# Kernel optimization log

Hardware: AMD Instinct MI355X
Metric: run time of the kernel (lower is better)

## Reference

```python
import jax, jax.numpy as jnp
import numpy as np

EPS = 1e-06

def _hermite_coeffs(coord_diff, sigmas):
    # coord_diff: [B,N,K,2], sigmas: [K] -> coeff: [B,N,K,6]
    dx = coord_diff[..., 0]  # [B,N,K]
    dy = coord_diff[..., 1]
    s2 = sigmas ** 2 + EPS   # [K], broadcasts over B,N
    s4 = sigmas ** 4 + EPS
    ones = jnp.ones_like(dx)
    # idx order follows nested (order, alpha) loop of the torch code:
    # (0,0), (0,1)->-dy, (1,0)->-dx, (0,2), (1,1), (2,0)
    coeff = jnp.stack([
        ones,
        -dy / s2,
        -dx / s2,
        dy ** 2 / s4 - 1.0 / s2,
        dx * dy / s4,
        dx ** 2 / s4 - 1.0 / s2,
    ], axis=-1)  # [B,N,K,6]
    return coeff


def setup_inputs() -> dict:
    key = jax.random.key(0)
    k1, k2, k3, k4, k5 = jax.random.split(key, 5)
    B, N, K, H, O = 4, 65536, 32, 6, 31
    return {
        "mlp_output": jax.random.normal(k1, (B, N, O), dtype=jnp.float32),
        "coord_diff": jax.random.normal(k2, (B, N, K, 2), dtype=jnp.float32),
        "sigmas": jax.random.uniform(k3, (K,), dtype=jnp.float32, minval=0.1, maxval=1.0),
        "gaussian_weights": jax.random.uniform(k4, (B, N, K), dtype=jnp.float32),
        "rbf_weights": jax.random.normal(k5, (K, H, O), dtype=jnp.float32),
    }


def reference(mlp_output, coord_diff, sigmas, gaussian_weights, rbf_weights):
    # final[b,n,o] = mlp_output[b,n,o] * sum_{k,h} coeff[b,n,k,h]*gw[b,n,k]*W[k,h,o]
    coeff = _hermite_coeffs(coord_diff, sigmas)            # [B,N,K,6]
    mix = jnp.einsum('bnkh,bnk,kho->bno', coeff, gaussian_weights, rbf_weights)
    return mlp_output * mix
```

## Files before the change

kernel.cpp:

```cpp
#include <hip/hip_runtime.h>

#define KK 32
#define HH 6
#define OO 31
#define EPS 1e-6f
#define PTS_BLK 256
#define V_DW (KK * 4 * HH * 8)

typedef float f32x16 __attribute__((ext_vector_type(16)));
typedef float f32x4  __attribute__((ext_vector_type(4)));

__device__ __align__(256) float V_dev[V_DW];

__global__ void hermite_prep_kernel(const float* __restrict__ W,
                                    const float* __restrict__ sigmas)
{
    int j = blockIdx.x * 256 + threadIdx.x;
    if (j >= V_DW) return;
    int k  = j / 192;
    int r  = j - k * 192;
    int oc = r / 48;
    int r2 = r - oc * 48;
    int h  = r2 >> 3;
    int o  = oc * 8 + (r2 & 7);
    float s  = sigmas[k];
    float s2 = s * s;
    float i2 = 1.0f / (s2 + EPS);
    float i4 = 1.0f / (s2 * s2 + EPS);
    float v = 0.0f;
    if (o < OO) {
        const float* Wk = W + k * (HH * OO);
        float w = Wk[h * OO + o];
        if (h == 0)      v = w - i2 * (Wk[3 * OO + o] + Wk[5 * OO + o]);
        else if (h <= 2) v = -i2 * w;
        else             v = i4 * w;
    }
    V_dev[j] = v;
}

#define CHUNK(PC, OCB)                                                     \
    {                                                                      \
        f32x16 t0, t1, t2;                                                 \
        asm volatile("s_load_dwordx16 %0, %3, 0x0\n\t"                     \
                     "s_load_dwordx16 %1, %3, 0x40\n\t"                    \
                     "s_load_dwordx16 %2, %3, 0x80\n\t"                    \
                     "s_waitcnt lgkmcnt(0)"                                \
                     : "=&s"(t0), "=&s"(t1), "=&s"(t2)                     \
                     : "s"(PC));                                           \
        _Pragma("unroll")                                                  \
        for (int o = 0; o < 8; ++o) {                                      \
            float a = acc[(OCB) + o];                                      \
            a = fmaf(g,  t0[o],     a);                                    \
            a = fmaf(d1, t0[8 + o], a);                                    \
            a = fmaf(d2, t1[o],     a);                                    \
            a = fmaf(d3, t1[8 + o], a);                                    \
            a = fmaf(d4, t2[o],     a);                                    \
            a = fmaf(d5, t2[8 + o], a);                                    \
            acc[(OCB) + o] = a;                                            \
        }                                                                  \
    }

#define JBLOCK(VS, GOFF)                                                   \
    _Pragma("unroll")                                                      \
    for (int j = 0; j < 8; ++j) {                                          \
        float dx = c[2 * j], dy = c[2 * j + 1];                            \
        float g  = ga[(GOFF) + j];                                         \
        float d1 = g * dy, d2 = g * dx;                                    \
        float d3 = d1 * dy, d4 = d1 * dx, d5 = d2 * dx;                    \
        const float* pk = (VS) + j * 192;                                  \
        CHUNK(pk,        0)                                                \
        CHUNK(pk + 48,   8)                                                \
        CHUNK(pk + 96,  16)                                                \
        CHUNK(pk + 144, 24)                                                \
    }

__global__ __launch_bounds__(256, 4) void hermite_fused_kernel(
    const float* __restrict__ mlp,
    const float* __restrict__ cd,
    const float* __restrict__ gw,
    float* __restrict__ out)
{
    __shared__ float smem[PTS_BLK * OO];

    const int tid = threadIdx.x;
    const int p   = blockIdx.x * PTS_BLK + tid;
    const float4* __restrict__ cdv = (const float4*)(cd + (size_t)p * (KK * 2));
    const float4* __restrict__ gwv = (const float4*)(gw + (size_t)p * KK);

    float acc[32];
#pragma unroll
    for (int o = 0; o < 32; ++o) acc[o] = 0.0f;

    const float* __restrict__ Vb = V_dev;

#pragma unroll 1
    for (int kt2 = 0; kt2 < 2; ++kt2) {
        float ga[16];
#pragma unroll
        for (int i = 0; i < 4; ++i) {
            float4 t = gwv[kt2 * 4 + i];
            ga[4 * i + 0] = t.x; ga[4 * i + 1] = t.y;
            ga[4 * i + 2] = t.z; ga[4 * i + 3] = t.w;
        }

        float c[16];
#pragma unroll
        for (int i = 0; i < 4; ++i) {
            float4 t = cdv[kt2 * 8 + i];
            c[4 * i + 0] = t.x; c[4 * i + 1] = t.y;
            c[4 * i + 2] = t.z; c[4 * i + 3] = t.w;
        }
        const float* Vs0 = Vb + (size_t)kt2 * (16 * 192);
        JBLOCK(Vs0, 0)

#pragma unroll
        for (int i = 0; i < 4; ++i) {
            float4 t = cdv[kt2 * 8 + 4 + i];
            c[4 * i + 0] = t.x; c[4 * i + 1] = t.y;
            c[4 * i + 2] = t.z; c[4 * i + 3] = t.w;
        }
        const float* Vs1 = Vs0 + 8 * 192;
        JBLOCK(Vs1, 8)
    }

#pragma unroll
    for (int o = 0; o < OO; ++o) smem[tid * OO + o] = acc[o];
    __syncthreads();

    {
        const size_t blk_dw = (size_t)blockIdx.x * (PTS_BLK * OO);
        const f32x4* __restrict__ mlpv = (const f32x4*)(mlp + blk_dw);
        f32x4* __restrict__ outv = (f32x4*)(out + blk_dw);
        const f32x4* mixv = (const f32x4*)smem;
#pragma unroll 2
        for (int j = tid; j < (PTS_BLK * OO) / 4; j += 256) {
            f32x4 m = __builtin_nontemporal_load(&mlpv[j]);
            f32x4 x = mixv[j];
            f32x4 r = m * x;
            __builtin_nontemporal_store(r, &outv[j]);
        }
    }
}

extern "C" void kernel_launch(void* const* d_in, const int* in_sizes, int n_in,
                              void* d_out, int out_size, void* d_ws, size_t ws_size,
                              hipStream_t stream)
{
    const float* mlp    = (const float*)d_in[0];
    const float* cd     = (const float*)d_in[1];
    const float* sigmas = (const float*)d_in[2];
    const float* gw     = (const float*)d_in[3];
    const float* W      = (const float*)d_in[4];
    float* out          = (float*)d_out;

    const int P = in_sizes[3] / KK;

    hermite_prep_kernel<<<(V_DW + 255) / 256, 256, 0, stream>>>(W, sigmas);
    hermite_fused_kernel<<<P / PTS_BLK, 256, 0, stream>>>(mlp, cd, gw, out);
}
```

Baseline: 199.3 us.

## Split output channels across waves so each wave handles four points per lane

Each wave now owns one 8-wide output-channel chunk of the precomputed weight table, and each lane computes four points instead of one. Each wave therefore issues only one set of 48 scalar loads per k and reuses them across four points, cutting scalar-load traffic and s_waitcnt stalls per FMA by about four times. In exchange every wave loads the coordinate and gaussian-weight inputs for all 256 points, so vector global reads rise roughly fourfold, though they should mostly hit in cache. The shared-memory write-out is remapped to the new point/channel layout.

Result: slower. 241.9 us (+21.3%).

```diff
diff --git a/kernel.cpp b/kernel.cpp
--- a/kernel.cpp
+++ b/kernel.cpp
@@ -38,42 +38,6 @@
     V_dev[j] = v;
 }
 
-#define CHUNK(PC, OCB)                                                     \
-    {                                                                      \
-        f32x16 t0, t1, t2;                                                 \
-        asm volatile("s_load_dwordx16 %0, %3, 0x0\n\t"                     \
-                     "s_load_dwordx16 %1, %3, 0x40\n\t"                    \
-                     "s_load_dwordx16 %2, %3, 0x80\n\t"                    \
-                     "s_waitcnt lgkmcnt(0)"                                \
-                     : "=&s"(t0), "=&s"(t1), "=&s"(t2)                     \
-                     : "s"(PC));                                           \
-        _Pragma("unroll")                                                  \
-        for (int o = 0; o < 8; ++o) {                                      \
-            float a = acc[(OCB) + o];                                      \
-            a = fmaf(g,  t0[o],     a);                                    \
-            a = fmaf(d1, t0[8 + o], a);                                    \
-            a = fmaf(d2, t1[o],     a);                                    \
-            a = fmaf(d3, t1[8 + o], a);                                    \
-            a = fmaf(d4, t2[o],     a);                                    \
-            a = fmaf(d5, t2[8 + o], a);                                    \
-            acc[(OCB) + o] = a;                                            \
-        }                                                                  \
-    }
-
-#define JBLOCK(VS, GOFF)                                                   \
-    _Pragma("unroll")                                                      \
-    for (int j = 0; j < 8; ++j) {                                          \
-        float dx = c[2 * j], dy = c[2 * j + 1];                            \
-        float g  = ga[(GOFF) + j];                                         \
-        float d1 = g * dy, d2 = g * dx;                                    \
-        float d3 = d1 * dy, d4 = d1 * dx, d5 = d2 * dx;                    \
-        const float* pk = (VS) + j * 192;                                  \
-        CHUNK(pk,        0)                                                \
-        CHUNK(pk + 48,   8)                                                \
-        CHUNK(pk + 96,  16)                                                \
-        CHUNK(pk + 144, 24)                                                \
-    }
-
 __global__ __launch_bounds__(256, 4) void hermite_fused_kernel(
     const float* __restrict__ mlp,
     const float* __restrict__ cd,
@@ -82,49 +46,82 @@
 {
     __shared__ float smem[PTS_BLK * OO];
 
-    const int tid = threadIdx.x;
-    const int p   = blockIdx.x * PTS_BLK + tid;
-    const float4* __restrict__ cdv = (const float4*)(cd + (size_t)p * (KK * 2));
-    const float4* __restrict__ gwv = (const float4*)(gw + (size_t)p * KK);
+    const int tid  = threadIdx.x;
+    const int lane = tid & 63;
+    const int wv   = tid >> 6;
+    const int p0   = blockIdx.x * PTS_BLK + lane;
+
+    const float4* __restrict__ cdv = (const float4*)(cd + (size_t)p0 * (KK * 2));
+    const float4* __restrict__ gwv = (const float4*)(gw + (size_t)p0 * KK);
 
     float acc[32];
 #pragma unroll
-    for (int o = 0; o < 32; ++o) acc[o] = 0.0f;
+    for (int i = 0; i < 32; ++i) acc[i] = 0.0f;
 
-    const float* __restrict__ Vb = V_dev;
+    const int wv_s = __builtin_amdgcn_readfirstlane(wv);
+    const float* Vw = V_dev + wv_s * 48;
 
 #pragma unroll 1
-    for (int kt2 = 0; kt2 < 2; ++kt2) {
-        float ga[16];
+    for (int kt = 0; kt < 4; ++kt) {
+        float ga[4][8];
 #pragma unroll
-        for (int i = 0; i < 4; ++i) {
-            float4 t = gwv[kt2 * 4 + i];
-            ga[4 * i + 0] = t.x; ga[4 * i + 1] = t.y;
-            ga[4 * i + 2] = t.z; ga[4 * i + 3] = t.w;
+        for (int m = 0; m < 4; ++m) {
+#pragma unroll
+            for (int i = 0; i < 2; ++i) {
+                float4 t = gwv[m * 512 + kt * 2 + i];
+                ga[m][4 * i + 0] = t.x; ga[m][4 * i + 1] = t.y;
+                ga[m][4 * i + 2] = t.z; ga[m][4 * i + 3] = t.w;
+            }
         }
-
-        float c[16];
 #pragma unroll
-        for (int i = 0; i < 4; ++i) {
-            float4 t = cdv[kt2 * 8 + i];
-            c[4 * i + 0] = t.x; c[4 * i + 1] = t.y;
-            c[4 * i + 2] = t.z; c[4 * i + 3] = t.w;
+        for (int jj = 0; jj < 4; ++jj) {
+            float c[4][4];
+#pragma unroll
+            for (int m = 0; m < 4; ++m) {
+                float4 t = cdv[m * 1024 + kt * 4 + jj];
+                c[m][0] = t.x; c[m][1] = t.y; c[m][2] = t.z; c[m][3] = t.w;
+            }
+#pragma unroll
+            for (int j2 = 0; j2 < 2; ++j2) {
+                const int k = kt * 8 + jj * 2 + j2;
+                const float* pk = Vw + k * 192;
+                f32x16 t0, t1, t2;
+                asm volatile("s_load_dwordx16 %0, %3, 0x0\n\t"
+                             "s_load_dwordx16 %1, %3, 0x40\n\t"
+                             "s_load_dwordx16 %2, %3, 0x80\n\t"
+                             "s_waitcnt lgkmcnt(0)"
+                             : "=&s"(t0), "=&s"(t1), "=&s"(t2)
+                             : "s"(pk));
+#pragma unroll
+                for (int m = 0; m < 4; ++m) {
+                    float dx = c[m][2 * j2], dy = c[m][2 * j2 + 1];
+                    float g  = ga[m][jj * 2 + j2];
+                    float d1 = g * dy, d2 = g * dx;
+                    float d3 = d1 * dy, d4 = d1 * dx, d5 = d2 * dx;
+#pragma unroll
+                    for (int o = 0; o < 8; ++o) {
+                        float a = acc[m * 8 + o];
+                        a = fmaf(g,  t0[o],     a);
+                        a = fmaf(d1, t0[8 + o], a);
+                        a = fmaf(d2, t1[o],     a);
+                        a = fmaf(d3, t1[8 + o], a);
+                        a = fmaf(d4, t2[o],     a);
+                        a = fmaf(d5, t2[8 + o], a);
+                        acc[m * 8 + o] = a;
+                    }
+                }
+            }
         }
-        const float* Vs0 = Vb + (size_t)kt2 * (16 * 192);
-        JBLOCK(Vs0, 0)
-
-#pragma unroll
-        for (int i = 0; i < 4; ++i) {
-            float4 t = cdv[kt2 * 8 + 4 + i];
-            c[4 * i + 0] = t.x; c[4 * i + 1] = t.y;
-            c[4 * i + 2] = t.z; c[4 * i + 3] = t.w;
-        }
-        const float* Vs1 = Vs0 + 8 * 192;
-        JBLOCK(Vs1, 8)
     }
 
 #pragma unroll
-    for (int o = 0; o < OO; ++o) smem[tid * OO + o] = acc[o];
+    for (int m = 0; m < 4; ++m) {
+#pragma unroll
+        for (int o = 0; o < 8; ++o) {
+            if (wv * 8 + o < OO)
+                smem[(m * 64 + lane) * OO + wv * 8 + o] = acc[m * 8 + o];
+        }
+    }
     __syncthreads();
 
     {
```
